# Optimization experiments

Hardware: AMD Instinct MI355X
Metric: run time of the kernel (lower is better)

Reference implementation:

```python
import jax, jax.numpy as jnp
import numpy as np

B, S, D, H = 2, 2048, 512, 8
DK = D // H
NEG = -1.0e9


def _xavier(key, shape):
    fan_in, fan_out = shape[-1], shape[0]
    lim = np.sqrt(6.0 / (fan_in + fan_out))
    return jax.random.uniform(key, shape, jnp.float32, -lim, lim)


def _rope_freqs(seq, dim):
    # lucidrains RotaryEmbedding: inv_freq over even dims, each freq repeated twice
    inv_freq = 1.0 / (10000.0 ** (jnp.arange(0, dim, 2, dtype=jnp.float32) / dim))
    freqs = jnp.arange(seq, dtype=jnp.float32)[:, None] * inv_freq[None, :]  # (S, dim/2)
    return jnp.repeat(freqs, 2, axis=-1)  # (S, dim)


def _rotate_half(x):
    xr = x.reshape(*x.shape[:-1], -1, 2)
    x1, x2 = xr[..., 0], xr[..., 1]
    return jnp.stack([-x2, x1], axis=-1).reshape(x.shape)


def _shift_down(s):
    # pad_zero row at position 0, drop last-but-keep rows 1: (concat trick)
    return jnp.concatenate([jnp.zeros_like(s[:, :, :1, :]), s[:, :, 1:, :]], axis=2)


def setup_inputs() -> dict:
    key = jax.random.key(0)
    kq, kk, kv, kt, kwq, kwk, kwv, kwo, kg = jax.random.split(key, 9)
    inp = {
        "q": jax.random.normal(kq, (B, S, D), jnp.float32),
        "k": jax.random.normal(kk, (B, S, D), jnp.float32),
        "v": jax.random.normal(kv, (B, S, D), jnp.float32),
        "ltime": jax.random.uniform(kt, (B, S), jnp.float32),
        "mask": jnp.broadcast_to(jnp.triu(jnp.ones((S, S), bool), k=1)[None], (B, S, S)),
        "Wq": _xavier(kwq, (D, D)), "bq": jnp.zeros((D,), jnp.float32),
        "Wk": _xavier(kwk, (D, D)), "bk": jnp.zeros((D,), jnp.float32),
        "Wv": _xavier(kwv, (D, D)), "bv": jnp.zeros((D,), jnp.float32),
        "Wo": _xavier(kwo, (D, D)), "bo": jnp.zeros((D,), jnp.float32),
        "gammas": jax.random.uniform(kg, (H, S, 1), jnp.float32, -0.1, 0.1),
    }
    return inp


def reference(q, k, v, ltime, mask, Wq, bq, Wk, bk, Wv, bv, Wo, bo, gammas):
    del ltime  # used only in dead code (dist_seq) in the original module

    def proj(x, W, b):
        return (x @ W.T + b).reshape(B, S, H, DK).transpose(0, 2, 1, 3)  # (B,H,S,DK)

    qh, kh, vh = proj(q, Wq, bq), proj(k, Wk, bk), proj(v, Wv, bv)

    freqs = _rope_freqs(S, DK)[None, None]  # (1,1,S,DK)
    cos, sin = jnp.cos(freqs), jnp.sin(freqs)
    qh = qh * cos + _rotate_half(qh) * sin
    kh = kh * cos + _rotate_half(kh) * sin

    scores = jnp.einsum("bhid,bhjd->bhij", qh, kh) / np.sqrt(DK)
    m = mask[:, None]  # (B,1,S,S)

    # --- no_grad distance-decay block ---
    s_ = jax.nn.softmax(jnp.where(m, NEG, scores), axis=-1)
    s_ = _shift_down(s_)
    distcum = jnp.cumsum(s_, axis=-1)
    disttot = jnp.sum(s_, axis=-1, keepdims=True)
    idx = jnp.arange(S, dtype=jnp.float32)
    pos_eff = jnp.abs(idx[None, :] - idx[:, None])[None, None]  # (1,1,S,S)
    dist = jax.lax.stop_gradient(
        jnp.sqrt(jnp.maximum((disttot - distcum) * pos_eff, 0.0)))

    g = -jax.nn.softplus(gammas)[None]  # (1,H,S,1)
    total_effect = jnp.clip(jnp.exp(dist * g), 1e-5, 1e5)
    scores = total_effect * scores

    scores = jax.nn.softmax(jnp.where(m, NEG, scores), axis=-1)
    scores = _shift_down(scores)

    out = jnp.einsum("bhij,bhjd->bhid", scores, vh)  # (B,H,S,DK)
    out = out.transpose(0, 2, 1, 3).reshape(B, S, D)
    return out @ Wo.T + bo
```

## Files before the change

### kernel.cpp

```cpp
#include <hip/hip_runtime.h>
#include <math.h>

#define B_ 2
#define S_ 2048
#define D_ 512
#define H_ 8
#define DK_ 64

typedef __attribute__((ext_vector_type(8))) short bf16x8;
typedef __attribute__((ext_vector_type(4))) float f32x4;

#define MFMA16(A, Bv, C) __builtin_amdgcn_mfma_f32_16x16x32_bf16(A, Bv, C, 0, 0, 0)

__device__ inline unsigned short f2bf(float x) {
  unsigned u = __float_as_uint(x);
  unsigned r = (u + 0x7fffu + ((u >> 16) & 1u)) >> 16;
  return (unsigned short)r;
}
__device__ inline unsigned pack2(float a, float b) {
  return (unsigned)f2bf(a) | ((unsigned)f2bf(b) << 16);
}

__global__ void rope_table_k(float* cs) {
  int idx = blockIdx.x * blockDim.x + threadIdx.x;
  if (idx >= S_ * 32) return;
  int s = idx >> 5, i = idx & 31;
  float invf = powf(10000.0f, -(float)(2 * i) / 64.0f);
  float ang = (float)s * invf;
  double a = (double)ang;
  cs[idx * 2]     = (float)cos(a);
  cs[idx * 2 + 1] = (float)sin(a);
}

__global__ __launch_bounds__(256)
void cvt3_k(const float* __restrict__ a, const float* __restrict__ b,
            const float* __restrict__ c, unsigned short* __restrict__ dst) {
  size_t idx = ((size_t)blockIdx.x * 256 + threadIdx.x) * 4;
  const size_t per = (size_t)4096 * 512;
  const float* src; size_t r;
  if (idx < per)            { src = a; r = idx; }
  else if (idx < 2 * per)   { src = b; r = idx - per; }
  else                      { src = c; r = idx - 2 * per; }
  float4 x = *(const float4*)(src + r);
  ushort4 y = { f2bf(x.x), f2bf(x.y), f2bf(x.z), f2bf(x.w) };
  *(ushort4*)(dst + idx) = y;
}
__global__ __launch_bounds__(256)
void cvt4_k(const float* __restrict__ a, const float* __restrict__ b,
            const float* __restrict__ c, const float* __restrict__ d,
            unsigned short* __restrict__ dst) {
  size_t idx = ((size_t)blockIdx.x * 256 + threadIdx.x) * 4;
  const size_t per = (size_t)512 * 512;
  const float* src; size_t r;
  if (idx < per)            { src = a; r = idx; }
  else if (idx < 2 * per)   { src = b; r = idx - per; }
  else if (idx < 3 * per)   { src = c; r = idx - 2 * per; }
  else                      { src = d; r = idx - 3 * per; }
  float4 x = *(const float4*)(src + r);
  ushort4 y = { f2bf(x.x), f2bf(x.y), f2bf(x.z), f2bf(x.w) };
  *(ushort4*)(dst + idx) = y;
}

__global__ __launch_bounds__(256)
void gemm_bf(const unsigned short* __restrict__ A,
             const unsigned short* __restrict__ W,
             const float* __restrict__ bias, void* __restrict__ Cout,
             const float* __restrict__ cs, int mode) {
  const int bm = blockIdx.y * 64, bn = blockIdx.x * 64;
  const int tid = threadIdx.x, w = tid >> 6, lane = tid & 63;
  const int li = lane & 15, lg = lane >> 4;
  __shared__ __align__(16) unsigned short As[64 * 64];
  __shared__ __align__(16) unsigned short Ws[64 * 64];
  f32x4 acc[4] = {{0.f,0.f,0.f,0.f},{0.f,0.f,0.f,0.f},{0.f,0.f,0.f,0.f},{0.f,0.f,0.f,0.f}};

  const int Bo0 = tid * 16, Bo1 = tid * 16 + 4096;
  const int r0 = Bo0 >> 7, c0 = Bo0 & 127;
  const int r1 = Bo1 >> 7, c1 = Bo1 & 127;
  const int so0 = (r0 * 128 + (c0 ^ ((r0 & 7) << 4))) >> 1;
  const int so1 = (r1 * 128 + (c1 ^ ((r1 & 7) << 4))) >> 1;

  const char* Abase = (const char*)A;
  const char* Wbase = (const char*)W;
  uint4 ra0 = *(const uint4*)(Abase + (size_t)(bm + r0) * 1024 + c0);
  uint4 ra1 = *(const uint4*)(Abase + (size_t)(bm + r1) * 1024 + c1);
  uint4 rw0 = *(const uint4*)(Wbase + (size_t)(bn + r0) * 1024 + c0);
  uint4 rw1 = *(const uint4*)(Wbase + (size_t)(bn + r1) * 1024 + c1);

  for (int t = 0; t < 8; ++t) {
    __syncthreads();
    *(uint4*)&As[so0] = ra0; *(uint4*)&As[so1] = ra1;
    *(uint4*)&Ws[so0] = rw0; *(uint4*)&Ws[so1] = rw1;
    __syncthreads();
    if (t < 7) {
      int k0 = (t + 1) * 128;
      ra0 = *(const uint4*)(Abase + (size_t)(bm + r0) * 1024 + k0 + c0);
      ra1 = *(const uint4*)(Abase + (size_t)(bm + r1) * 1024 + k0 + c1);
      rw0 = *(const uint4*)(Wbase + (size_t)(bn + r0) * 1024 + k0 + c0);
      rw1 = *(const uint4*)(Wbase + (size_t)(bn + r1) * 1024 + k0 + c1);
    }
#pragma unroll
    for (int kk = 0; kk < 2; ++kk) {
      const int brow = w * 16 + li;
      bf16x8 bf = *(const bf16x8*)&Ws[brow * 64 + (((kk * 64 + lg * 16) ^ ((brow & 7) << 4)) >> 1)];
#pragma unroll
      for (int mt = 0; mt < 4; ++mt) {
        const int arow = mt * 16 + li;
        bf16x8 af = *(const bf16x8*)&As[arow * 64 + (((kk * 64 + lg * 16) ^ ((arow & 7) << 4)) >> 1)];
        acc[mt] = MFMA16(af, bf, acc[mt]);
      }
    }
  }

  const int n = bn + w * 16 + li;
  const float bv = bias[n];
  if (mode == 0) {
    float* C = (float*)Cout;
#pragma unroll
    for (int mt = 0; mt < 4; ++mt)
#pragma unroll
      for (int r = 0; r < 4; ++r) {
        int m = bm + mt * 16 + lg * 4 + r;
        C[(size_t)m * 512 + n] = acc[mt][r] + bv;
      }
  } else if (mode == 1) {
    unsigned short* C = (unsigned short*)Cout;
    const int d = n & 63, hh = n >> 6, p = d >> 1;
#pragma unroll
    for (int mt = 0; mt < 4; ++mt)
#pragma unroll
      for (int r = 0; r < 4; ++r) {
        int m = bm + mt * 16 + lg * 4 + r;
        int bb = m >> 11, sp = m & (S_ - 1);
        float val = acc[mt][r] + bv;
        float other = __shfl_xor(val, 1, 64);
        const float* cp = cs + ((size_t)sp * 32 + p) * 2;
        float cc = cp[0], sn = cp[1];
        float y = (d & 1) ? (val * cc + other * sn) : (val * cc - other * sn);
        C[(((size_t)bb * H_ + hh) * S_ + sp) * DK_ + d] = f2bf(y);
      }
  } else {
    unsigned short* C = (unsigned short*)Cout;
    const int d = n & 63, hh = n >> 6;
#pragma unroll
    for (int mt = 0; mt < 4; ++mt) {
      int m0 = bm + mt * 16 + lg * 4;
      int bb = m0 >> 11, sp0 = m0 & (S_ - 1);
      ushort4 y = { f2bf(acc[mt][0] + bv), f2bf(acc[mt][1] + bv),
                    f2bf(acc[mt][2] + bv), f2bf(acc[mt][3] + bv) };
      *(ushort4*)&C[(((size_t)bb * H_ + hh) * DK_ + d) * S_ + sp0] = y;
    }
  }
}

__global__ __launch_bounds__(256)
void attn3(const unsigned short* __restrict__ Qbf,
           const unsigned short* __restrict__ Kbf,
           const unsigned short* __restrict__ Vtbf,
           const float* __restrict__ gammas,
           unsigned short* __restrict__ out_pre) {
  const int qt = 127 - (int)blockIdx.x;
  const int bh = blockIdx.y;
  const int h = bh & (H_ - 1), b = bh >> 3;
  const int i0 = qt * 16;
  const int tid = threadIdx.x;
  const int w = tid >> 6, lane = tid & 63;
  const int li = lane & 15, lg = lane >> 4;
  const int i = i0 + li;

  __shared__ __align__(16) unsigned short P[4][16][40];
  __shared__ float sm1[4][16], sden[4][16], sm2[4][16], sl2[4][16];
  __shared__ float Obuf[4][64][17];

  const unsigned short* Qp = Qbf + (size_t)bh * (S_ * DK_);
  const unsigned short* Kp = Kbf + (size_t)bh * (S_ * DK_);
  const unsigned short* Vp = Vtbf + (size_t)bh * (DK_ * S_);

  bf16x8 qb0 = *(const bf16x8*)(Qp + (size_t)i * DK_ + lg * 8);
  bf16x8 qb1 = *(const bf16x8*)(Qp + (size_t)i * DK_ + 32 + lg * 8);

  const int ntile = (i0 >> 5) + 1;
  const int nt4 = (ntile + 3) >> 2;
  const int tb = (w * nt4 < ntile) ? w * nt4 : ntile;
  const int te = (tb + nt4 < ntile) ? tb + nt4 : ntile;

  const float g = -log1pf(__expf(gammas[h * S_ + i]));

  float m1w = -INFINITY, denw = 0.f;
  bf16x8 ka0, ka1, ka2, ka3;
  if (tb < te) {
    const int jb = tb * 32;
    const unsigned short* p0 = Kp + (size_t)(jb + li) * DK_ + lg * 8;
    const unsigned short* p1 = Kp + (size_t)(jb + 16 + li) * DK_ + lg * 8;
    ka0 = *(const bf16x8*)p0; ka1 = *(const bf16x8*)(p0 + 32);
    ka2 = *(const bf16x8*)p1; ka3 = *(const bf16x8*)(p1 + 32);
  }
  for (int t = tb; t < te; ++t) {
    const int j0 = t * 32;
    const bool pf = (t + 1 < te);
    bf16x8 na0, na1, na2, na3;
    if (pf) {
      const unsigned short* p0 = Kp + (size_t)(j0 + 32 + li) * DK_ + lg * 8;
      const unsigned short* p1 = Kp + (size_t)(j0 + 48 + li) * DK_ + lg * 8;
      na0 = *(const bf16x8*)p0; na1 = *(const bf16x8*)(p0 + 32);
      na2 = *(const bf16x8*)p1; na3 = *(const bf16x8*)(p1 + 32);
    }
    f32x4 acc0 = {0.f,0.f,0.f,0.f}, acc1 = {0.f,0.f,0.f,0.f};
    acc0 = MFMA16(ka0, qb0, acc0); acc0 = MFMA16(ka1, qb1, acc0);
    acc1 = MFMA16(ka2, qb0, acc1); acc1 = MFMA16(ka3, qb1, acc1);
    float sv[8]; float mloc = -INFINITY;
#pragma unroll
    for (int x = 0; x < 8; ++x) {
      float s = ((x < 4) ? acc0[x & 3] : acc1[x & 3]) * 0.125f;
      sv[x] = s;
      int j = j0 + ((x >> 2) << 4) + lg * 4 + (x & 3);
      mloc = fmaxf(mloc, (j <= i) ? s : -INFINITY);
    }
    mloc = fmaxf(mloc, __shfl_xor(mloc, 16, 64));
    mloc = fmaxf(mloc, __shfl_xor(mloc, 32, 64));
    float mn = fmaxf(m1w, mloc);
    float sc = __expf(m1w - mn);
    float ls = 0.f;
#pragma unroll
    for (int x = 0; x < 8; ++x) {
      int j = j0 + ((x >> 2) << 4) + lg * 4 + (x & 3);
      ls += (j <= i) ? __expf(sv[x] - mn) : 0.f;
    }
    ls += __shfl_xor(ls, 16, 64);
    ls += __shfl_xor(ls, 32, 64);
    denw = denw * sc + ls;
    m1w = mn;
    if (pf) { ka0 = na0; ka1 = na1; ka2 = na2; ka3 = na3; }
  }
  if (lg == 0) { sm1[w][li] = m1w; sden[w][li] = denw; }
  __syncthreads();

  const float gm0 = sm1[0][li], gm1v = sm1[1][li], gm2v = sm1[2][li], gm3v = sm1[3][li];
  const float m1 = fmaxf(fmaxf(gm0, gm1v), fmaxf(gm2v, gm3v));
  const float d0 = sden[0][li] * __expf(gm0 - m1);
  const float d1 = sden[1][li] * __expf(gm1v - m1);
  const float d2 = sden[2][li] * __expf(gm2v - m1);
  const float d3 = sden[3][li] * __expf(gm3v - m1);
  const float den = d0 + d1 + d2 + d3;
  const float inv1 = 1.f / den;
  float cum = 0.f;
  if (w > 0) cum += d0;
  if (w > 1) cum += d1;
  if (w > 2) cum += d2;

  float m2w = -INFINITY, l2w = 0.f;
  f32x4 o0 = {0.f,0.f,0.f,0.f}, o1 = {0.f,0.f,0.f,0.f};
  f32x4 o2 = {0.f,0.f,0.f,0.f}, o3 = {0.f,0.f,0.f,0.f};
  bf16x8 va0, va1, va2, va3;
  if (tb < te) {
    const int jb = tb * 32;
    const unsigned short* p0 = Kp + (size_t)(jb + li) * DK_ + lg * 8;
    const unsigned short* p1 = Kp + (size_t)(jb + 16 + li) * DK_ + lg * 8;
    ka0 = *(const bf16x8*)p0; ka1 = *(const bf16x8*)(p0 + 32);
    ka2 = *(const bf16x8*)p1; ka3 = *(const bf16x8*)(p1 + 32);
    va0 = *(const bf16x8*)(Vp + (size_t)li * S_ + jb + lg * 8);
    va1 = *(const bf16x8*)(Vp + (size_t)(16 + li) * S_ + jb + lg * 8);
    va2 = *(const bf16x8*)(Vp + (size_t)(32 + li) * S_ + jb + lg * 8);
    va3 = *(const bf16x8*)(Vp + (size_t)(48 + li) * S_ + jb + lg * 8);
  }
  for (int t = tb; t < te; ++t) {
    const int j0 = t * 32;
    const bool pf = (t + 1 < te);
    bf16x8 na0, na1, na2, na3, nv0, nv1, nv2, nv3;
    if (pf) {
      const int j1 = j0 + 32;
      const unsigned short* p0 = Kp + (size_t)(j1 + li) * DK_ + lg * 8;
      const unsigned short* p1 = Kp + (size_t)(j1 + 16 + li) * DK_ + lg * 8;
      na0 = *(const bf16x8*)p0; na1 = *(const bf16x8*)(p0 + 32);
      na2 = *(const bf16x8*)p1; na3 = *(const bf16x8*)(p1 + 32);
      nv0 = *(const bf16x8*)(Vp + (size_t)li * S_ + j1 + lg * 8);
      nv1 = *(const bf16x8*)(Vp + (size_t)(16 + li) * S_ + j1 + lg * 8);
      nv2 = *(const bf16x8*)(Vp + (size_t)(32 + li) * S_ + j1 + lg * 8);
      nv3 = *(const bf16x8*)(Vp + (size_t)(48 + li) * S_ + j1 + lg * 8);
    }
    f32x4 acc0 = {0.f,0.f,0.f,0.f}, acc1 = {0.f,0.f,0.f,0.f};
    acc0 = MFMA16(ka0, qb0, acc0); acc0 = MFMA16(ka1, qb1, acc0);
    acc1 = MFMA16(ka2, qb0, acc1); acc1 = MFMA16(ka3, qb1, acc1);

    float sv[8], ev[8]; bool uv[8];
#pragma unroll
    for (int x = 0; x < 8; ++x) {
      float s = ((x < 4) ? acc0[x & 3] : acc1[x & 3]) * 0.125f;
      sv[x] = s;
      int j = j0 + ((x >> 2) << 4) + lg * 4 + (x & 3);
      uv[x] = (j <= i);
      ev[x] = uv[x] ? __expf(s - m1) : 0.f;
    }
    float L0 = ev[0] + ev[1] + ev[2] + ev[3];
    float L1 = ev[4] + ev[5] + ev[6] + ev[7];
    float v0 = L0;
    { float tt = __shfl_up(v0, 16, 64); if (lg >= 1) v0 += tt;
      tt = __shfl_up(v0, 32, 64); if (lg >= 2) v0 += tt; }
    float tot0 = __shfl(v0, li + 48, 64);
    float v1 = L1;
    { float tt = __shfl_up(v1, 16, 64); if (lg >= 1) v1 += tt;
      tt = __shfl_up(v1, 32, 64); if (lg >= 2) v1 += tt; }
    float tot1 = __shfl(v1, li + 48, 64);
    float base0 = cum + (v0 - L0);
    float base1 = cum + tot0 + (v1 - L1);
    cum += tot0 + tot1;

    float s2[8]; float run = base0;
#pragma unroll
    for (int x = 0; x < 8; ++x) {
      if (x == 4) run = base1;
      run += ev[x];
      int j = j0 + ((x >> 2) << 4) + lg * 4 + (x & 3);
      float rem = fmaxf(1.f - run * inv1, 0.f);
      float dist = sqrtf(fmaxf(rem * (float)(i - j), 0.f));
      float te2 = fminf(fmaxf(__expf(dist * g), 1e-5f), 1e5f);
      s2[x] = uv[x] ? te2 * sv[x] : -INFINITY;
    }
    float mloc = s2[0];
#pragma unroll
    for (int x = 1; x < 8; ++x) mloc = fmaxf(mloc, s2[x]);
    mloc = fmaxf(mloc, __shfl_xor(mloc, 16, 64));
    mloc = fmaxf(mloc, __shfl_xor(mloc, 32, 64));
    float mn = fmaxf(m2w, mloc);
    float f = __expf(m2w - mn);
    float p[8]; float ls = 0.f;
#pragma unroll
    for (int x = 0; x < 8; ++x) { p[x] = __expf(s2[x] - mn); ls += p[x]; }
    ls += __shfl_xor(ls, 16, 64);
    ls += __shfl_xor(ls, 32, 64);
    l2w = l2w * f + ls;
    m2w = mn;
    o0 *= f; o1 *= f; o2 *= f; o3 *= f;

    { uint2 w0v = { pack2(p[0], p[1]), pack2(p[2], p[3]) };
      uint2 w1v = { pack2(p[4], p[5]), pack2(p[6], p[7]) };
      *(uint2*)&P[w][li][lg * 4] = w0v;
      *(uint2*)&P[w][li][16 + lg * 4] = w1v; }
    bf16x8 pb = *(const bf16x8*)&P[w][li][lg * 8];
    o0 = MFMA16(va0, pb, o0);
    o1 = MFMA16(va1, pb, o1);
    o2 = MFMA16(va2, pb, o2);
    o3 = MFMA16(va3, pb, o3);

    if (pf) { ka0 = na0; ka1 = na1; ka2 = na2; ka3 = na3;
              va0 = nv0; va1 = nv1; va2 = nv2; va3 = nv3; }
  }

  if (lg == 0) { sm2[w][li] = m2w; sl2[w][li] = l2w; }
  {
    f32x4 oo[4] = { o0, o1, o2, o3 };
#pragma unroll
    for (int db = 0; db < 4; ++db)
#pragma unroll
      for (int e = 0; e < 4; ++e)
        Obuf[w][lane][db * 4 + e] = oo[db][e];
  }
  __syncthreads();
  if (w == 0) {
    const float q0 = sm2[0][li], q1 = sm2[1][li], q2 = sm2[2][li], q3 = sm2[3][li];
    const float m2 = fmaxf(fmaxf(q0, q1), fmaxf(q2, q3));
    const float f0 = __expf(q0 - m2), f1 = __expf(q1 - m2);
    const float f2 = __expf(q2 - m2), f3 = __expf(q3 - m2);
    const float l2 = sl2[0][li] * f0 + sl2[1][li] * f1 + sl2[2][li] * f2 + sl2[3][li] * f3;
    const float z = (i == 0) ? 0.f : (1.f / l2);
    unsigned short* dst = out_pre + ((size_t)(b * S_ + i)) * D_ + h * DK_;
#pragma unroll
    for (int db = 0; db < 4; ++db) {
      float vo[4];
#pragma unroll
      for (int e = 0; e < 4; ++e)
        vo[e] = (Obuf[0][lane][db * 4 + e] * f0 + Obuf[1][lane][db * 4 + e] * f1 +
                 Obuf[2][lane][db * 4 + e] * f2 + Obuf[3][lane][db * 4 + e] * f3) * z;
      ushort4 y = { f2bf(vo[0]), f2bf(vo[1]), f2bf(vo[2]), f2bf(vo[3]) };
      *(ushort4*)&dst[db * 16 + lg * 4] = y;
    }
  }
}

extern "C" void kernel_launch(void* const* d_in, const int* in_sizes, int n_in,
                              void* d_out, int out_size, void* d_ws, size_t ws_size,
                              hipStream_t stream) {
  const float* q  = (const float*)d_in[0];
  const float* k  = (const float*)d_in[1];
  const float* v  = (const float*)d_in[2];
  const float* Wq = (const float*)d_in[5];
  const float* bq = (const float*)d_in[6];
  const float* Wk = (const float*)d_in[7];
  const float* bk = (const float*)d_in[8];
  const float* Wv = (const float*)d_in[9];
  const float* bv = (const float*)d_in[10];
  const float* Wo = (const float*)d_in[11];
  const float* bo = (const float*)d_in[12];
  const float* gammas = (const float*)d_in[13];
  float* out = (float*)d_out;

  float* cs = (float*)d_ws;
  unsigned short* Abf  = (unsigned short*)(cs + (size_t)S_ * 32 * 2);
  unsigned short* Wbf  = Abf + (size_t)3 * 4096 * 512;
  unsigned short* Qbf  = Wbf + (size_t)4 * 512 * 512;
  unsigned short* Kbf  = Qbf + (size_t)B_ * H_ * S_ * DK_;
  unsigned short* Vtbf = Kbf + (size_t)B_ * H_ * S_ * DK_;
  unsigned short* out_pre = Vtbf + (size_t)B_ * H_ * S_ * DK_;

  rope_table_k<<<(S_ * 32 + 255) / 256, 256, 0, stream>>>(cs);
  cvt3_k<<<6144, 256, 0, stream>>>(q, k, v, Abf);
  cvt4_k<<<1024, 256, 0, stream>>>(Wq, Wk, Wv, Wo, Wbf);

  const size_t nA = (size_t)4096 * 512;
  const size_t nW = (size_t)512 * 512;
  dim3 gg(8, 64);
  gemm_bf<<<gg, 256, 0, stream>>>(Abf,          Wbf,          bq, Qbf,  cs, 1);
  gemm_bf<<<gg, 256, 0, stream>>>(Abf + nA,     Wbf + nW,     bk, Kbf,  cs, 1);
  gemm_bf<<<gg, 256, 0, stream>>>(Abf + 2 * nA, Wbf + 2 * nW, bv, Vtbf, cs, 2);

  attn3<<<dim3(128, B_ * H_), 256, 0, stream>>>(Qbf, Kbf, Vtbf, gammas, out_pre);

  gemm_bf<<<gg, 256, 0, stream>>>(out_pre, Wbf + 3 * nW, bo, out, cs, 0);
}
```

Baseline: 285.5 us.

## Double-buffer GEMM via direct LDS loads, batch QKV launches, pair attention tiles

The GEMM now stages A/W tiles straight from global memory into double-buffered LDS with global_load_lds, so the next k-tile loads while the current one is computed. The three projection GEMMs are merged into one launch that uses blockIdx.z. The attention kernel processes two query tiles per block, a long one (127-bx) and a short one (bx), to even out the causal workload, and the grid is halved. Attention also switches from __expf to exp2 with log2e folded into the scale, and the final output reduction is spread across all four waves instead of one. The costs are more LDS per GEMM block, fewer attention blocks in flight, and extra barriers.

```diff
diff --git a/kernel.cpp b/kernel.cpp
--- a/kernel.cpp
+++ b/kernel.cpp
@@ -11,6 +11,8 @@
 typedef __attribute__((ext_vector_type(4))) float f32x4;
 
 #define MFMA16(A, Bv, C) __builtin_amdgcn_mfma_f32_16x16x32_bf16(A, Bv, C, 0, 0, 0)
+#define EXP2(x) __builtin_amdgcn_exp2f(x)
+#define LOG2E 1.4426950408889634f
 
 __device__ inline unsigned short f2bf(float x) {
   unsigned u = __float_as_uint(x);
@@ -19,6 +21,10 @@
 }
 __device__ inline unsigned pack2(float a, float b) {
   return (unsigned)f2bf(a) | ((unsigned)f2bf(b) << 16);
+}
+__device__ __forceinline__ void gload16(const void* g, void* l) {
+  __builtin_amdgcn_global_load_lds((const __attribute__((address_space(1))) unsigned*)g,
+                                   (__attribute__((address_space(3))) unsigned*)l, 16, 0, 0);
 }
 
 __global__ void rope_table_k(float* cs) {
@@ -61,54 +67,52 @@
   *(ushort4*)(dst + idx) = y;
 }
 
-__global__ __launch_bounds__(256)
-void gemm_bf(const unsigned short* __restrict__ A,
-             const unsigned short* __restrict__ W,
-             const float* __restrict__ bias, void* __restrict__ Cout,
-             const float* __restrict__ cs, int mode) {
+__device__ __forceinline__ void gemm64_core(
+    const unsigned short* __restrict__ A, const unsigned short* __restrict__ W,
+    const float* __restrict__ bias, void* __restrict__ Cout,
+    const float* __restrict__ cs, int mode,
+    unsigned short (*As)[64 * 64], unsigned short (*Ws)[64 * 64]) {
   const int bm = blockIdx.y * 64, bn = blockIdx.x * 64;
   const int tid = threadIdx.x, w = tid >> 6, lane = tid & 63;
   const int li = lane & 15, lg = lane >> 4;
-  __shared__ __align__(16) unsigned short As[64 * 64];
-  __shared__ __align__(16) unsigned short Ws[64 * 64];
-  f32x4 acc[4] = {{0.f,0.f,0.f,0.f},{0.f,0.f,0.f,0.f},{0.f,0.f,0.f,0.f},{0.f,0.f,0.f,0.f}};
-
-  const int Bo0 = tid * 16, Bo1 = tid * 16 + 4096;
-  const int r0 = Bo0 >> 7, c0 = Bo0 & 127;
-  const int r1 = Bo1 >> 7, c1 = Bo1 & 127;
-  const int so0 = (r0 * 128 + (c0 ^ ((r0 & 7) << 4))) >> 1;
-  const int so1 = (r1 * 128 + (c1 ^ ((r1 & 7) << 4))) >> 1;
-
-  const char* Abase = (const char*)A;
-  const char* Wbase = (const char*)W;
-  uint4 ra0 = *(const uint4*)(Abase + (size_t)(bm + r0) * 1024 + c0);
-  uint4 ra1 = *(const uint4*)(Abase + (size_t)(bm + r1) * 1024 + c1);
-  uint4 rw0 = *(const uint4*)(Wbase + (size_t)(bn + r0) * 1024 + c0);
-  uint4 rw1 = *(const uint4*)(Wbase + (size_t)(bn + r1) * 1024 + c1);
-
+  f32x4 acc[4] = {};
+
+  const char* Ab0 = (const char*)A + (size_t)bm * 1024;
+  const char* Wb0 = (const char*)W + (size_t)bn * 1024;
+
+  auto stage = [&](int buf, int t) {
+    const char* Ab = Ab0 + t * 128;
+    const char* Wb = Wb0 + t * 128;
+    char* AsB = (char*)&As[buf][0];
+    char* WsB = (char*)&Ws[buf][0];
+#pragma unroll
+    for (int rr = 0; rr < 2; ++rr) {
+      const int rowbase = rr * 32 + w * 8;
+      const int row = rowbase + (lane >> 3);
+      const int sc_ = ((lane & 7) ^ (row & 7)) << 4;
+      gload16(Ab + (size_t)row * 1024 + sc_, AsB + rowbase * 128);
+      gload16(Wb + (size_t)row * 1024 + sc_, WsB + rowbase * 128);
+    }
+  };
+
+  stage(0, 0);
+  int cur = 0;
   for (int t = 0; t < 8; ++t) {
     __syncthreads();
-    *(uint4*)&As[so0] = ra0; *(uint4*)&As[so1] = ra1;
-    *(uint4*)&Ws[so0] = rw0; *(uint4*)&Ws[so1] = rw1;
-    __syncthreads();
-    if (t < 7) {
-      int k0 = (t + 1) * 128;
-      ra0 = *(const uint4*)(Abase + (size_t)(bm + r0) * 1024 + k0 + c0);
-      ra1 = *(const uint4*)(Abase + (size_t)(bm + r1) * 1024 + k0 + c1);
-      rw0 = *(const uint4*)(Wbase + (size_t)(bn + r0) * 1024 + k0 + c0);
-      rw1 = *(const uint4*)(Wbase + (size_t)(bn + r1) * 1024 + k0 + c1);
-    }
+    if (t < 7) stage(cur ^ 1, t + 1);
 #pragma unroll
     for (int kk = 0; kk < 2; ++kk) {
+      const int chunk = kk * 4 + lg;
       const int brow = w * 16 + li;
-      bf16x8 bf = *(const bf16x8*)&Ws[brow * 64 + (((kk * 64 + lg * 16) ^ ((brow & 7) << 4)) >> 1)];
+      bf16x8 bf = *(const bf16x8*)&Ws[cur][brow * 64 + ((chunk ^ (brow & 7)) << 3)];
 #pragma unroll
       for (int mt = 0; mt < 4; ++mt) {
         const int arow = mt * 16 + li;
-        bf16x8 af = *(const bf16x8*)&As[arow * 64 + (((kk * 64 + lg * 16) ^ ((arow & 7) << 4)) >> 1)];
+        bf16x8 af = *(const bf16x8*)&As[cur][arow * 64 + ((chunk ^ (arow & 7)) << 3)];
         acc[mt] = MFMA16(af, bf, acc[mt]);
       }
     }
+    cur ^= 1;
   }
 
   const int n = bn + w * 16 + li;
@@ -153,19 +157,45 @@
 }
 
 __global__ __launch_bounds__(256)
+void gemm_proj(const unsigned short* __restrict__ Abf,
+               const unsigned short* __restrict__ Wbf,
+               const float* __restrict__ bq, const float* __restrict__ bk,
+               const float* __restrict__ bv,
+               unsigned short* __restrict__ Qbf, unsigned short* __restrict__ Kbf,
+               unsigned short* __restrict__ Vtbf, const float* __restrict__ cs) {
+  __shared__ __align__(16) unsigned short As[2][64 * 64];
+  __shared__ __align__(16) unsigned short Ws[2][64 * 64];
+  const int z = blockIdx.z;
+  const size_t nA = (size_t)4096 * 512, nW = (size_t)512 * 512;
+  const unsigned short* A = Abf + (size_t)z * nA;
+  const unsigned short* W = Wbf + (size_t)z * nW;
+  const float* bias = (z == 0) ? bq : (z == 1) ? bk : bv;
+  void* out = (z == 0) ? (void*)Qbf : (z == 1) ? (void*)Kbf : (void*)Vtbf;
+  const int mode = (z == 2) ? 2 : 1;
+  gemm64_core(A, W, bias, out, cs, mode, As, Ws);
+}
+
+__global__ __launch_bounds__(256)
+void gemm_one(const unsigned short* __restrict__ A, const unsigned short* __restrict__ W,
+              const float* __restrict__ bias, float* __restrict__ out) {
+  __shared__ __align__(16) unsigned short As[2][64 * 64];
+  __shared__ __align__(16) unsigned short Ws[2][64 * 64];
+  gemm64_core(A, W, bias, out, nullptr, 0, As, Ws);
+}
+
+__global__ __launch_bounds__(256)
 void attn3(const unsigned short* __restrict__ Qbf,
            const unsigned short* __restrict__ Kbf,
            const unsigned short* __restrict__ Vtbf,
            const float* __restrict__ gammas,
            unsigned short* __restrict__ out_pre) {
-  const int qt = 127 - (int)blockIdx.x;
+  const int bx = (int)blockIdx.x;
   const int bh = blockIdx.y;
   const int h = bh & (H_ - 1), b = bh >> 3;
-  const int i0 = qt * 16;
   const int tid = threadIdx.x;
   const int w = tid >> 6, lane = tid & 63;
   const int li = lane & 15, lg = lane >> 4;
-  const int i = i0 + li;
+  const float SCL = 0.125f * LOG2E;
 
   __shared__ __align__(16) unsigned short P[4][16][40];
   __shared__ float sm1[4][16], sden[4][16], sm2[4][16], sl2[4][16];
@@ -175,204 +205,208 @@
   const unsigned short* Kp = Kbf + (size_t)bh * (S_ * DK_);
   const unsigned short* Vp = Vtbf + (size_t)bh * (DK_ * S_);
 
-  bf16x8 qb0 = *(const bf16x8*)(Qp + (size_t)i * DK_ + lg * 8);
-  bf16x8 qb1 = *(const bf16x8*)(Qp + (size_t)i * DK_ + 32 + lg * 8);
-
-  const int ntile = (i0 >> 5) + 1;
-  const int nt4 = (ntile + 3) >> 2;
-  const int tb = (w * nt4 < ntile) ? w * nt4 : ntile;
-  const int te = (tb + nt4 < ntile) ? tb + nt4 : ntile;
-
-  const float g = -log1pf(__expf(gammas[h * S_ + i]));
-
-  float m1w = -INFINITY, denw = 0.f;
-  bf16x8 ka0, ka1, ka2, ka3;
-  if (tb < te) {
-    const int jb = tb * 32;
-    const unsigned short* p0 = Kp + (size_t)(jb + li) * DK_ + lg * 8;
-    const unsigned short* p1 = Kp + (size_t)(jb + 16 + li) * DK_ + lg * 8;
-    ka0 = *(const bf16x8*)p0; ka1 = *(const bf16x8*)(p0 + 32);
-    ka2 = *(const bf16x8*)p1; ka3 = *(const bf16x8*)(p1 + 32);
-  }
-  for (int t = tb; t < te; ++t) {
-    const int j0 = t * 32;
-    const bool pf = (t + 1 < te);
-    bf16x8 na0, na1, na2, na3;
-    if (pf) {
-      const unsigned short* p0 = Kp + (size_t)(j0 + 32 + li) * DK_ + lg * 8;
-      const unsigned short* p1 = Kp + (size_t)(j0 + 48 + li) * DK_ + lg * 8;
-      na0 = *(const bf16x8*)p0; na1 = *(const bf16x8*)(p0 + 32);
-      na2 = *(const bf16x8*)p1; na3 = *(const bf16x8*)(p1 + 32);
-    }
-    f32x4 acc0 = {0.f,0.f,0.f,0.f}, acc1 = {0.f,0.f,0.f,0.f};
-    acc0 = MFMA16(ka0, qb0, acc0); acc0 = MFMA16(ka1, qb1, acc0);
-    acc1 = MFMA16(ka2, qb0, acc1); acc1 = MFMA16(ka3, qb1, acc1);
-    float sv[8]; float mloc = -INFINITY;
-#pragma unroll
-    for (int x = 0; x < 8; ++x) {
-      float s = ((x < 4) ? acc0[x & 3] : acc1[x & 3]) * 0.125f;
-      sv[x] = s;
-      int j = j0 + ((x >> 2) << 4) + lg * 4 + (x & 3);
-      mloc = fmaxf(mloc, (j <= i) ? s : -INFINITY);
-    }
-    mloc = fmaxf(mloc, __shfl_xor(mloc, 16, 64));
-    mloc = fmaxf(mloc, __shfl_xor(mloc, 32, 64));
-    float mn = fmaxf(m1w, mloc);
-    float sc = __expf(m1w - mn);
-    float ls = 0.f;
-#pragma unroll
-    for (int x = 0; x < 8; ++x) {
-      int j = j0 + ((x >> 2) << 4) + lg * 4 + (x & 3);
-      ls += (j <= i) ? __expf(sv[x] - mn) : 0.f;
-    }
-    ls += __shfl_xor(ls, 16, 64);
-    ls += __shfl_xor(ls, 32, 64);
-    denw = denw * sc + ls;
-    m1w = mn;
-    if (pf) { ka0 = na0; ka1 = na1; ka2 = na2; ka3 = na3; }
-  }
-  if (lg == 0) { sm1[w][li] = m1w; sden[w][li] = denw; }
-  __syncthreads();
-
-  const float gm0 = sm1[0][li], gm1v = sm1[1][li], gm2v = sm1[2][li], gm3v = sm1[3][li];
-  const float m1 = fmaxf(fmaxf(gm0, gm1v), fmaxf(gm2v, gm3v));
-  const float d0 = sden[0][li] * __expf(gm0 - m1);
-  const float d1 = sden[1][li] * __expf(gm1v - m1);
-  const float d2 = sden[2][li] * __expf(gm2v - m1);
-  const float d3 = sden[3][li] * __expf(gm3v - m1);
-  const float den = d0 + d1 + d2 + d3;
-  const float inv1 = 1.f / den;
-  float cum = 0.f;
-  if (w > 0) cum += d0;
-  if (w > 1) cum += d1;
-  if (w > 2) cum += d2;
-
-  float m2w = -INFINITY, l2w = 0.f;
-  f32x4 o0 = {0.f,0.f,0.f,0.f}, o1 = {0.f,0.f,0.f,0.f};
-  f32x4 o2 = {0.f,0.f,0.f,0.f}, o3 = {0.f,0.f,0.f,0.f};
-  bf16x8 va0, va1, va2, va3;
-  if (tb < te) {
-    const int jb = tb * 32;
-    const unsigned short* p0 = Kp + (size_t)(jb + li) * DK_ + lg * 8;
-    const unsigned short* p1 = Kp + (size_t)(jb + 16 + li) * DK_ + lg * 8;
-    ka0 = *(const bf16x8*)p0; ka1 = *(const bf16x8*)(p0 + 32);
-    ka2 = *(const bf16x8*)p1; ka3 = *(const bf16x8*)(p1 + 32);
-    va0 = *(const bf16x8*)(Vp + (size_t)li * S_ + jb + lg * 8);
-    va1 = *(const bf16x8*)(Vp + (size_t)(16 + li) * S_ + jb + lg * 8);
-    va2 = *(const bf16x8*)(Vp + (size_t)(32 + li) * S_ + jb + lg * 8);
-    va3 = *(const bf16x8*)(Vp + (size_t)(48 + li) * S_ + jb + lg * 8);
-  }
-  for (int t = tb; t < te; ++t) {
-    const int j0 = t * 32;
-    const bool pf = (t + 1 < te);
-    bf16x8 na0, na1, na2, na3, nv0, nv1, nv2, nv3;
-    if (pf) {
-      const int j1 = j0 + 32;
-      const unsigned short* p0 = Kp + (size_t)(j1 + li) * DK_ + lg * 8;
-      const unsigned short* p1 = Kp + (size_t)(j1 + 16 + li) * DK_ + lg * 8;
-      na0 = *(const bf16x8*)p0; na1 = *(const bf16x8*)(p0 + 32);
-      na2 = *(const bf16x8*)p1; na3 = *(const bf16x8*)(p1 + 32);
-      nv0 = *(const bf16x8*)(Vp + (size_t)li * S_ + j1 + lg * 8);
-      nv1 = *(const bf16x8*)(Vp + (size_t)(16 + li) * S_ + j1 + lg * 8);
-      nv2 = *(const bf16x8*)(Vp + (size_t)(32 + li) * S_ + j1 + lg * 8);
-      nv3 = *(const bf16x8*)(Vp + (size_t)(48 + li) * S_ + j1 + lg * 8);
-    }
-    f32x4 acc0 = {0.f,0.f,0.f,0.f}, acc1 = {0.f,0.f,0.f,0.f};
-    acc0 = MFMA16(ka0, qb0, acc0); acc0 = MFMA16(ka1, qb1, acc0);
-    acc1 = MFMA16(ka2, qb0, acc1); acc1 = MFMA16(ka3, qb1, acc1);
-
-    float sv[8], ev[8]; bool uv[8];
-#pragma unroll
-    for (int x = 0; x < 8; ++x) {
-      float s = ((x < 4) ? acc0[x & 3] : acc1[x & 3]) * 0.125f;
-      sv[x] = s;
-      int j = j0 + ((x >> 2) << 4) + lg * 4 + (x & 3);
-      uv[x] = (j <= i);
-      ev[x] = uv[x] ? __expf(s - m1) : 0.f;
-    }
-    float L0 = ev[0] + ev[1] + ev[2] + ev[3];
-    float L1 = ev[4] + ev[5] + ev[6] + ev[7];
-    float v0 = L0;
-    { float tt = __shfl_up(v0, 16, 64); if (lg >= 1) v0 += tt;
-      tt = __shfl_up(v0, 32, 64); if (lg >= 2) v0 += tt; }
-    float tot0 = __shfl(v0, li + 48, 64);
-    float v1 = L1;
-    { float tt = __shfl_up(v1, 16, 64); if (lg >= 1) v1 += tt;
-      tt = __shfl_up(v1, 32, 64); if (lg >= 2) v1 += tt; }
-    float tot1 = __shfl(v1, li + 48, 64);
-    float base0 = cum + (v0 - L0);
-    float base1 = cum + tot0 + (v1 - L1);
-    cum += tot0 + tot1;
-
-    float s2[8]; float run = base0;
-#pragma unroll
-    for (int x = 0; x < 8; ++x) {
-      if (x == 4) run = base1;
-      run += ev[x];
-      int j = j0 + ((x >> 2) << 4) + lg * 4 + (x & 3);
-      float rem = fmaxf(1.f - run * inv1, 0.f);
-      float dist = sqrtf(fmaxf(rem * (float)(i - j), 0.f));
-      float te2 = fminf(fmaxf(__expf(dist * g), 1e-5f), 1e5f);
-      s2[x] = uv[x] ? te2 * sv[x] : -INFINITY;
-    }
-    float mloc = s2[0];
-#pragma unroll
-    for (int x = 1; x < 8; ++x) mloc = fmaxf(mloc, s2[x]);
-    mloc = fmaxf(mloc, __shfl_xor(mloc, 16, 64));
-    mloc = fmaxf(mloc, __shfl_xor(mloc, 32, 64));
-    float mn = fmaxf(m2w, mloc);
-    float f = __expf(m2w - mn);
-    float p[8]; float ls = 0.f;
-#pragma unroll
-    for (int x = 0; x < 8; ++x) { p[x] = __expf(s2[x] - mn); ls += p[x]; }
-    ls += __shfl_xor(ls, 16, 64);
-    ls += __shfl_xor(ls, 32, 64);
-    l2w = l2w * f + ls;
-    m2w = mn;
-    o0 *= f; o1 *= f; o2 *= f; o3 *= f;
-
-    { uint2 w0v = { pack2(p[0], p[1]), pack2(p[2], p[3]) };
-      uint2 w1v = { pack2(p[4], p[5]), pack2(p[6], p[7]) };
-      *(uint2*)&P[w][li][lg * 4] = w0v;
-      *(uint2*)&P[w][li][16 + lg * 4] = w1v; }
-    bf16x8 pb = *(const bf16x8*)&P[w][li][lg * 8];
-    o0 = MFMA16(va0, pb, o0);
-    o1 = MFMA16(va1, pb, o1);
-    o2 = MFMA16(va2, pb, o2);
-    o3 = MFMA16(va3, pb, o3);
-
-    if (pf) { ka0 = na0; ka1 = na1; ka2 = na2; ka3 = na3;
-              va0 = nv0; va1 = nv1; va2 = nv2; va3 = nv3; }
-  }
-
-  if (lg == 0) { sm2[w][li] = m2w; sl2[w][li] = l2w; }
-  {
-    f32x4 oo[4] = { o0, o1, o2, o3 };
-#pragma unroll
-    for (int db = 0; db < 4; ++db)
+  for (int half = 0; half < 2; ++half) {
+    const int qt = half ? bx : (127 - bx);
+    const int i0 = qt * 16;
+    const int i = i0 + li;
+
+    bf16x8 qb0 = *(const bf16x8*)(Qp + (size_t)i * DK_ + lg * 8);
+    bf16x8 qb1 = *(const bf16x8*)(Qp + (size_t)i * DK_ + 32 + lg * 8);
+
+    const int ntile = (i0 >> 5) + 1;
+    const int nt4 = (ntile + 3) >> 2;
+    const int tb = (w * nt4 < ntile) ? w * nt4 : ntile;
+    const int te = (tb + nt4 < ntile) ? tb + nt4 : ntile;
+
+    const float g2 = -log1pf(__expf(gammas[h * S_ + i])) * LOG2E;
+
+    float m1w = -INFINITY, denw = 0.f;
+    bf16x8 ka0, ka1, ka2, ka3;
+    if (tb < te) {
+      const int jb = tb * 32;
+      const unsigned short* p0 = Kp + (size_t)(jb + li) * DK_ + lg * 8;
+      const unsigned short* p1 = Kp + (size_t)(jb + 16 + li) * DK_ + lg * 8;
+      ka0 = *(const bf16x8*)p0; ka1 = *(const bf16x8*)(p0 + 32);
+      ka2 = *(const bf16x8*)p1; ka3 = *(const bf16x8*)(p1 + 32);
+    }
+    for (int t = tb; t < te; ++t) {
+      const int j0 = t * 32;
+      const bool pf = (t + 1 < te);
+      bf16x8 na0, na1, na2, na3;
+      if (pf) {
+        const unsigned short* p0 = Kp + (size_t)(j0 + 32 + li) * DK_ + lg * 8;
+        const unsigned short* p1 = Kp + (size_t)(j0 + 48 + li) * DK_ + lg * 8;
+        na0 = *(const bf16x8*)p0; na1 = *(const bf16x8*)(p0 + 32);
+        na2 = *(const bf16x8*)p1; na3 = *(const bf16x8*)(p1 + 32);
+      }
+      f32x4 acc0 = {0.f,0.f,0.f,0.f}, acc1 = {0.f,0.f,0.f,0.f};
+      acc0 = MFMA16(ka0, qb0, acc0); acc0 = MFMA16(ka1, qb1, acc0);
+      acc1 = MFMA16(ka2, qb0, acc1); acc1 = MFMA16(ka3, qb1, acc1);
+      float sv[8]; float mloc = -INFINITY;
+#pragma unroll
+      for (int x = 0; x < 8; ++x) {
+        float s = ((x < 4) ? acc0[x & 3] : acc1[x & 3]) * SCL;
+        sv[x] = s;
+        int j = j0 + ((x >> 2) << 4) + lg * 4 + (x & 3);
+        mloc = fmaxf(mloc, (j <= i) ? s : -INFINITY);
+      }
+      mloc = fmaxf(mloc, __shfl_xor(mloc, 16, 64));
+      mloc = fmaxf(mloc, __shfl_xor(mloc, 32, 64));
+      float mn = fmaxf(m1w, mloc);
+      float sc = EXP2(m1w - mn);
+      float ls = 0.f;
+#pragma unroll
+      for (int x = 0; x < 8; ++x) {
+        int j = j0 + ((x >> 2) << 4) + lg * 4 + (x & 3);
+        ls += (j <= i) ? EXP2(sv[x] - mn) : 0.f;
+      }
+      ls += __shfl_xor(ls, 16, 64);
+      ls += __shfl_xor(ls, 32, 64);
+      denw = denw * sc + ls;
+      m1w = mn;
+      if (pf) { ka0 = na0; ka1 = na1; ka2 = na2; ka3 = na3; }
+    }
+    if (lg == 0) { sm1[w][li] = m1w; sden[w][li] = denw; }
+    __syncthreads();
+
+    const float gm0 = sm1[0][li], gm1v = sm1[1][li], gm2v = sm1[2][li], gm3v = sm1[3][li];
+    const float m1 = fmaxf(fmaxf(gm0, gm1v), fmaxf(gm2v, gm3v));
+    const float d0 = sden[0][li] * EXP2(gm0 - m1);
+    const float d1 = sden[1][li] * EXP2(gm1v - m1);
+    const float d2 = sden[2][li] * EXP2(gm2v - m1);
+    const float d3 = sden[3][li] * EXP2(gm3v - m1);
+    const float den = d0 + d1 + d2 + d3;
+    const float inv1 = 1.f / den;
+    float cum = 0.f;
+    if (w > 0) cum += d0;
+    if (w > 1) cum += d1;
+    if (w > 2) cum += d2;
+
+    float m2w = -INFINITY, l2w = 0.f;
+    f32x4 o0 = {0.f,0.f,0.f,0.f}, o1 = {0.f,0.f,0.f,0.f};
+    f32x4 o2 = {0.f,0.f,0.f,0.f}, o3 = {0.f,0.f,0.f,0.f};
+    bf16x8 va0, va1, va2, va3;
+    if (tb < te) {
+      const int jb = tb * 32;
+      const unsigned short* p0 = Kp + (size_t)(jb + li) * DK_ + lg * 8;
+      const unsigned short* p1 = Kp + (size_t)(jb + 16 + li) * DK_ + lg * 8;
+      ka0 = *(const bf16x8*)p0; ka1 = *(const bf16x8*)(p0 + 32);
+      ka2 = *(const bf16x8*)p1; ka3 = *(const bf16x8*)(p1 + 32);
+      va0 = *(const bf16x8*)(Vp + (size_t)li * S_ + jb + lg * 8);
+      va1 = *(const bf16x8*)(Vp + (size_t)(16 + li) * S_ + jb + lg * 8);
+      va2 = *(const bf16x8*)(Vp + (size_t)(32 + li) * S_ + jb + lg * 8);
+      va3 = *(const bf16x8*)(Vp + (size_t)(48 + li) * S_ + jb + lg * 8);
+    }
+    for (int t = tb; t < te; ++t) {
+      const int j0 = t * 32;
+      const bool pf = (t + 1 < te);
+      bf16x8 na0, na1, na2, na3, nv0, nv1, nv2, nv3;
+      if (pf) {
+        const int j1 = j0 + 32;
+        const unsigned short* p0 = Kp + (size_t)(j1 + li) * DK_ + lg * 8;
+        const unsigned short* p1 = Kp + (size_t)(j1 + 16 + li) * DK_ + lg * 8;
+        na0 = *(const bf16x8*)p0; na1 = *(const bf16x8*)(p0 + 32);
+        na2 = *(const bf16x8*)p1; na3 = *(const bf16x8*)(p1 + 32);
+        nv0 = *(const bf16x8*)(Vp + (size_t)li * S_ + j1 + lg * 8);
+        nv1 = *(const bf16x8*)(Vp + (size_t)(16 + li) * S_ + j1 + lg * 8);
+        nv2 = *(const bf16x8*)(Vp + (size_t)(32 + li) * S_ + j1 + lg * 8);
+        nv3 = *(const bf16x8*)(Vp + (size_t)(48 + li) * S_ + j1 + lg * 8);
+      }
+      f32x4 acc0 = {0.f,0.f,0.f,0.f}, acc1 = {0.f,0.f,0.f,0.f};
+      acc0 = MFMA16(ka0, qb0, acc0); acc0 = MFMA16(ka1, qb1, acc0);
+      acc1 = MFMA16(ka2, qb0, acc1); acc1 = MFMA16(ka3, qb1, acc1);
+
+      float sv[8], ev[8]; bool uv[8];
+#pragma unroll
+      for (int x = 0; x < 8; ++x) {
+        float s = ((x < 4) ? acc0[x & 3] : acc1[x & 3]) * SCL;
+        sv[x] = s;
+        int j = j0 + ((x >> 2) << 4) + lg * 4 + (x & 3);
+        uv[x] = (j <= i);
+        ev[x] = uv[x] ? EXP2(s - m1) : 0.f;
+      }
+      float L0 = ev[0] + ev[1] + ev[2] + ev[3];
+      float L1 = ev[4] + ev[5] + ev[6] + ev[7];
+      float v0 = L0;
+      { float tt = __shfl_up(v0, 16, 64); if (lg >= 1) v0 += tt;
+        tt = __shfl_up(v0, 32, 64); if (lg >= 2) v0 += tt; }
+      float tot0 = __shfl(v0, li + 48, 64);
+      float v1 = L1;
+      { float tt = __shfl_up(v1, 16, 64); if (lg >= 1) v1 += tt;
+        tt = __shfl_up(v1, 32, 64); if (lg >= 2) v1 += tt; }
+      float tot1 = __shfl(v1, li + 48, 64);
+      float base0 = cum + (v0 - L0);
+      float base1 = cum + tot0 + (v1 - L1);
+      cum += tot0 + tot1;
+
+      float s2[8]; float run = base0;
+#pragma unroll
+      for (int x = 0; x < 8; ++x) {
+        if (x == 4) run = base1;
+        run += ev[x];
+        int j = j0 + ((x >> 2) << 4) + lg * 4 + (x & 3);
+        float rem = fmaxf(1.f - run * inv1, 0.f);
+        float dist = sqrtf(fmaxf(rem * (float)(i - j), 0.f));
+        float te2 = fminf(fmaxf(EXP2(dist * g2), 1e-5f), 1e5f);
+        s2[x] = uv[x] ? te2 * sv[x] : -INFINITY;
+      }
+      float mloc = s2[0];
+#pragma unroll
+      for (int x = 1; x < 8; ++x) mloc = fmaxf(mloc, s2[x]);
+      mloc = fmaxf(mloc, __shfl_xor(mloc, 16, 64));
+      mloc = fmaxf(mloc, __shfl_xor(mloc, 32, 64));
+      float mn = fmaxf(m2w, mloc);
+      float f = EXP2(m2w - mn);
+      float p[8]; float ls = 0.f;
+#pragma unroll
+      for (int x = 0; x < 8; ++x) { p[x] = EXP2(s2[x] - mn); ls += p[x]; }
+      ls += __shfl_xor(ls, 16, 64);
+      ls += __shfl_xor(ls, 32, 64);
+      l2w = l2w * f + ls;
+      m2w = mn;
+      o0 *= f; o1 *= f; o2 *= f; o3 *= f;
+
+      { uint2 w0v = { pack2(p[0], p[1]), pack2(p[2], p[3]) };
+        uint2 w1v = { pack2(p[4], p[5]), pack2(p[6], p[7]) };
+        *(uint2*)&P[w][li][lg * 4] = w0v;
+        *(uint2*)&P[w][li][16 + lg * 4] = w1v; }
+      bf16x8 pb = *(const bf16x8*)&P[w][li][lg * 8];
+      o0 = MFMA16(va0, pb, o0);
+      o1 = MFMA16(va1, pb, o1);
+      o2 = MFMA16(va2, pb, o2);
+      o3 = MFMA16(va3, pb, o3);
+
+      if (pf) { ka0 = na0; ka1 = na1; ka2 = na2; ka3 = na3;
+                va0 = nv0; va1 = nv1; va2 = nv2; va3 = nv3; }
+    }
+
+    if (lg == 0) { sm2[w][li] = m2w; sl2[w][li] = l2w; }
+    {
+      f32x4 oo[4] = { o0, o1, o2, o3 };
+#pragma unroll
+      for (int db = 0; db < 4; ++db)
+#pragma unroll
+        for (int e = 0; e < 4; ++e)
+          Obuf[w][lane][db * 4 + e] = oo[db][e];
+    }
+    __syncthreads();
+    {
+      const float q0 = sm2[0][li], q1 = sm2[1][li], q2 = sm2[2][li], q3 = sm2[3][li];
+      const float m2 = fmaxf(fmaxf(q0, q1), fmaxf(q2, q3));
+      const float f0 = EXP2(q0 - m2), f1 = EXP2(q1 - m2);
+      const float f2 = EXP2(q2 - m2), f3 = EXP2(q3 - m2);
+      const float l2 = sl2[0][li] * f0 + sl2[1][li] * f1 + sl2[2][li] * f2 + sl2[3][li] * f3;
+      const float z = (i == 0) ? 0.f : (1.f / l2);
+      unsigned short* dst = out_pre + ((size_t)(b * S_ + i)) * D_ + h * DK_;
+      float vo[4];
 #pragma unroll
       for (int e = 0; e < 4; ++e)
-        Obuf[w][lane][db * 4 + e] = oo[db][e];
-  }
-  __syncthreads();
-  if (w == 0) {
-    const float q0 = sm2[0][li], q1 = sm2[1][li], q2 = sm2[2][li], q3 = sm2[3][li];
-    const float m2 = fmaxf(fmaxf(q0, q1), fmaxf(q2, q3));
-    const float f0 = __expf(q0 - m2), f1 = __expf(q1 - m2);
-    const float f2 = __expf(q2 - m2), f3 = __expf(q3 - m2);
-    const float l2 = sl2[0][li] * f0 + sl2[1][li] * f1 + sl2[2][li] * f2 + sl2[3][li] * f3;
-    const float z = (i == 0) ? 0.f : (1.f / l2);
-    unsigned short* dst = out_pre + ((size_t)(b * S_ + i)) * D_ + h * DK_;
-#pragma unroll
-    for (int db = 0; db < 4; ++db) {
-      float vo[4];
-#pragma unroll
-      for (int e = 0; e < 4; ++e)
-        vo[e] = (Obuf[0][lane][db * 4 + e] * f0 + Obuf[1][lane][db * 4 + e] * f1 +
-                 Obuf[2][lane][db * 4 + e] * f2 + Obuf[3][lane][db * 4 + e] * f3) * z;
+        vo[e] = (Obuf[0][lane][w * 4 + e] * f0 + Obuf[1][lane][w * 4 + e] * f1 +
+                 Obuf[2][lane][w * 4 + e] * f2 + Obuf[3][lane][w * 4 + e] * f3) * z;
       ushort4 y = { f2bf(vo[0]), f2bf(vo[1]), f2bf(vo[2]), f2bf(vo[3]) };
-      *(ushort4*)&dst[db * 16 + lg * 4] = y;
-    }
+      *(ushort4*)&dst[w * 16 + lg * 4] = y;
+    }
+    __syncthreads();
   }
 }
 
@@ -405,14 +439,10 @@
   cvt3_k<<<6144, 256, 0, stream>>>(q, k, v, Abf);
   cvt4_k<<<1024, 256, 0, stream>>>(Wq, Wk, Wv, Wo, Wbf);
 
-  const size_t nA = (size_t)4096 * 512;
   const size_t nW = (size_t)512 * 512;
-  dim3 gg(8, 64);
-  gemm_bf<<<gg, 256, 0, stream>>>(Abf,          Wbf,          bq, Qbf,  cs, 1);
-  gemm_bf<<<gg, 256, 0, stream>>>(Abf + nA,     Wbf + nW,     bk, Kbf,  cs, 1);
-  gemm_bf<<<gg, 256, 0, stream>>>(Abf + 2 * nA, Wbf + 2 * nW, bv, Vtbf, cs, 2);
-
-  attn3<<<dim3(128, B_ * H_), 256, 0, stream>>>(Qbf, Kbf, Vtbf, gammas, out_pre);
-
-  gemm_bf<<<gg, 256, 0, stream>>>(out_pre, Wbf + 3 * nW, bo, out, cs, 0);
-}
+  gemm_proj<<<dim3(8, 64, 3), 256, 0, stream>>>(Abf, Wbf, bq, bk, bv, Qbf, Kbf, Vtbf, cs);
+
+  attn3<<<dim3(64, B_ * H_), 256, 0, stream>>>(Qbf, Kbf, Vtbf, gammas, out_pre);
+
+  gemm_one<<<dim3(8, 64), 256, 0, stream>>>(out_pre, Wbf + 3 * nW, bo, out);
+}
```

Measured after the change: 256.7 us. -10.1%, faster.
